# Kernel tuning notes

Hardware: AMD Instinct MI355X
Metric: run time of the kernel (lower is better)

Reference implementation:

```python
import jax, jax.numpy as jnp
import numpy as np
from jax import lax

S = 30      # num_sensors
FD = 200    # feature_dim
T = 1024    # signal length
B = 1024    # batch
NC = 7      # num_classes


def setup_inputs() -> dict:
    key = jax.random.key(0)
    ks = jax.random.split(key, 24)
    rn = lambda i, shape: jax.random.normal(ks[i], shape, jnp.float32) * 0.05
    # normalized adjacency with self-loops: D^-1/2 (A+I) D^-1/2
    rng = np.random.default_rng(0)
    A = (rng.random((S, S)) > 0.7).astype(np.float32)
    A = ((A + A.T) > 0).astype(np.float32)
    A_self = A + np.eye(S, dtype=np.float32)
    dinv = 1.0 / np.sqrt(A_self.sum(1))
    adj_self = jnp.asarray(dinv[:, None] * A_self * dinv[None, :])
    return dict(
        x=jax.random.normal(ks[0], (B, S, T), jnp.float32),
        adj_self=adj_self,
        Wc1=rn(1, (S, S, 3)), bc1=jnp.zeros((S,), jnp.float32),
        Wc2=rn(2, (S, S, 3)), bc2=jnp.zeros((S,), jnp.float32),
        Wt=rn(3, (T, FD)), bt=jnp.zeros((FD,), jnp.float32),
        Wa=rn(4, (FD, FD)),
        Wm1=rn(5, (FD, FD)), Wm2=rn(6, (FD, FD)), Wm3=rn(7, (FD, FD)),
        Wg1=rn(8, (FD, FD)), Wg2=rn(9, (FD, FD)),
        wg=rn(10, (FD, 3)),
        Wp1=rn(11, (FD, FD // 2)), Wp2=rn(12, (FD, FD // 2)), Wp3=rn(13, (FD, FD // 2)),
        Wl=rn(14, (FD, 150)), Wgl=rn(15, (FD, 150)),
        Ws1=rn(16, (S, S // 2)), Ws2=rn(17, (S // 2, S)),
        Wf1=rn(18, (300, 150)), Wf2=rn(19, (150, 300)),
        Wcls=rn(20, (S * 600, NC)), bcls=jnp.zeros((NC,), jnp.float32),
    )


def reference(x, adj_self, Wc1, bc1, Wc2, bc2, Wt, bt, Wa, Wm1, Wm2, Wm3,
              Wg1, Wg2, wg, Wp1, Wp2, Wp3, Wl, Wgl, Ws1, Ws2, Wf1, Wf2,
              Wcls, bcls):
    dn = ('NCH', 'OIH', 'NCH')
    # CNN feature extractor: [B,S,T] -> [B,S,FD]
    h = jax.nn.relu(lax.conv_general_dilated(x, Wc1, (1,), 'SAME', dimension_numbers=dn) + bc1[None, :, None])
    h = jax.nn.relu(lax.conv_general_dilated(h, Wc2, (1,), 'SAME', dimension_numbers=dn) + bc2[None, :, None])
    F2 = jax.nn.relu(jnp.einsum('bst,tf->bsf', h, Wt) + bt)
    # MGCN: learned feature adjacency + 3-order GCN (batched, replaces per-sample loop)
    A_F = jax.nn.softmax(jax.nn.relu(jnp.einsum('bif,fg,bjg->bij', F2, Wa, F2)), axis=-1)
    gc = lambda A, X, W: jax.nn.relu(jnp.einsum('bij,bjf,fg->big', A, X, W))
    x1 = gc(A_F, F2, Wm1)
    x2 = gc(A_F, x1, Wm2)
    x3 = gc(A_F, x2, Wm3)
    # signal GCN on physical adjacency (2-layer, eval mode so dropout is identity)
    h1 = jax.nn.relu(jnp.einsum('ij,bjf,fg->big', adj_self, F2, Wg1))
    x_sensor = jnp.einsum('ij,bjf,fg->big', adj_self, h1, Wg2)
    H1 = (x1 + x_sensor) * 0.5
    H2 = (x2 + x_sensor) * 0.5
    H3 = (x3 + x_sensor) * 0.5
    # adaptive aggregation: per-node softmax gate over 3 branches, project to FD//2 each -> 300
    scores = jnp.stack([jnp.einsum('bsf,f->bs', H, wg[:, k]) for k, H in enumerate((H1, H2, H3))], -1)
    g = jax.nn.softmax(scores, -1)  # [B,S,3]
    agg = lambda k, H, Wp: jnp.einsum('ij,bjf,fg->big', adj_self, g[..., k:k + 1] * H, Wp)
    G_h = jnp.concatenate([agg(0, H1, Wp1), agg(1, H2, Wp2), agg(2, H3, Wp3)], -1)  # [B,S,300]
    # LGFM: local (physical adj) + global (learned adj) -> 150+150
    loc = jax.nn.relu(jnp.einsum('ij,bjf,fg->big', adj_self, F2, Wl))
    glb = jax.nn.relu(jnp.einsum('bij,bjf,fg->big', A_F, F2, Wgl))
    G_v = jnp.concatenate([loc, glb], -1)  # [B,S,300]
    # cross squeeze-excitation: channel SE on G_h driven by G_v, feature SE on G_v driven by G_h
    wch = jax.nn.sigmoid(jax.nn.relu(G_v.mean(-1) @ Ws1) @ Ws2)   # [B,S]
    G_h_att = G_h * wch[:, :, None]
    wft = jax.nn.sigmoid(jax.nn.relu(G_h.mean(1) @ Wf1) @ Wf2)    # [B,300]
    G_v_att = G_v * wft[:, None, :]
    G = jnp.concatenate([G_h_att, G_v_att], -1).reshape(x.shape[0], -1)  # [B, S*600]
    return jax.nn.log_softmax(G @ Wcls + bcls, axis=-1)
```

## Files before the change

kernel.cpp:

```cpp
#include <hip/hip_runtime.h>
#include <math.h>

#define S   30
#define FD  200
#define TT  1024
#define BB  1024
#define NC  7

#define OFS_C1   0ull
#define OFS_F2   31457280ull
#define OFS_AF   0ull
#define OFS_GV   921600ull
#define OFS_GH   10137600ull
#define OFS_WCH  19353600ull
#define OFS_WFT  19384320ull
#define OFS_R    19691520ull

__global__ __launch_bounds__(256) void k_conv1(
    const float* __restrict__ x,
    const float* __restrict__ Wc1, const float* __restrict__ bc1,
    float* __restrict__ C1) {
    const int c = blockIdx.x, b = blockIdx.y;
    const int t = threadIdx.x;
    const int t0 = c * 256;
    __shared__ float xb[S * 258];
    __shared__ float w1l[90 * 32];
    for (int idx = t; idx < 2700; idx += 256) {
        int so = idx / 90, r = idx % 90;
        w1l[r * 32 + so] = Wc1[idx];
    }
    for (int idx = t; idx < 180; idx += 256) {
        int r = idx >> 1, z = idx & 1;
        w1l[r * 32 + 30 + z] = 0.f;
    }
    for (int idx = t; idx < S * 64; idx += 256) {
        int s = idx >> 6, u = idx & 63;
        float4 v = *(const float4*)(x + (size_t)(b * S + s) * TT + t0 + 4 * u);
        float* d = xb + s * 258 + 1 + 4 * u;
        d[0] = v.x; d[1] = v.y; d[2] = v.z; d[3] = v.w;
    }
    if (t < 60) {
        int s = t % S;
        if (t < S) {
            int gt = t0 - 1;
            xb[s * 258] = (gt >= 0) ? x[(size_t)(b * S + s) * TT + gt] : 0.f;
        } else {
            int gt = t0 + 256;
            xb[s * 258 + 257] = (gt < TT) ? x[(size_t)(b * S + s) * TT + gt] : 0.f;
        }
    }
    __syncthreads();
    float acc[32];
#pragma unroll
    for (int so = 0; so < 32; so++) acc[so] = (so < S) ? bc1[so] : 0.f;
    for (int si = 0; si < S; si++) {
        float v0 = xb[si * 258 + t];
        float v1 = xb[si * 258 + t + 1];
        float v2 = xb[si * 258 + t + 2];
        const float* wr = w1l + si * 96;
#pragma unroll
        for (int u = 0; u < 8; u++) {
            float4 w0 = *(const float4*)(wr + 4 * u);
            float4 w1 = *(const float4*)(wr + 32 + 4 * u);
            float4 w2 = *(const float4*)(wr + 64 + 4 * u);
            acc[4 * u + 0] = fmaf(w0.x, v0, fmaf(w1.x, v1, fmaf(w2.x, v2, acc[4 * u + 0])));
            acc[4 * u + 1] = fmaf(w0.y, v0, fmaf(w1.y, v1, fmaf(w2.y, v2, acc[4 * u + 1])));
            acc[4 * u + 2] = fmaf(w0.z, v0, fmaf(w1.z, v1, fmaf(w2.z, v2, acc[4 * u + 2])));
            acc[4 * u + 3] = fmaf(w0.w, v0, fmaf(w1.w, v1, fmaf(w2.w, v2, acc[4 * u + 3])));
        }
    }
#pragma unroll
    for (int so = 0; so < 32; so++) {
        if (so < S)
            C1[(size_t)(b * S + so) * TT + t0 + t] = fmaxf(acc[so], 0.f);
    }
}

#define FMA4(av, wv, accm)                           \
    {                                                \
        accm[0] = fmaf(av, (wv).x, accm[0]);         \
        accm[1] = fmaf(av, (wv).y, accm[1]);         \
        accm[2] = fmaf(av, (wv).z, accm[2]);         \
        accm[3] = fmaf(av, (wv).w, accm[3]);         \
    }

__device__ inline void fma_tile8(const float4 a0, const float4 a1,
                                 const float4 w[8], float accm[4]) {
    FMA4(a0.x, w[0], accm); FMA4(a0.y, w[1], accm);
    FMA4(a0.z, w[2], accm); FMA4(a0.w, w[3], accm);
    FMA4(a1.x, w[4], accm); FMA4(a1.y, w[5], accm);
    FMA4(a1.z, w[6], accm); FMA4(a1.w, w[7], accm);
}

template<int RPT>
__device__ inline void zacc(float acc[][4]) {
#pragma unroll
    for (int m = 0; m < RPT; m++)
#pragma unroll
        for (int q = 0; q < 4; q++) acc[m][q] = 0.f;
}

template<int RPT, int N, int K>
__device__ inline void gemm_w4_pf(const float* Xl, int xstr, const float* __restrict__ W,
                                  int ct, int rt, float acc[][4]) {
    const float* wp = W + 4 * ct;
    float4 wreg[8];
#pragma unroll
    for (int u = 0; u < 8; u++) wreg[u] = *(const float4*)(wp + u * N);
#pragma unroll 1
    for (int kt = 0; kt < K / 8 - 1; kt++) {
        float4 wnxt[8];
#pragma unroll
        for (int u = 0; u < 8; u++) wnxt[u] = *(const float4*)(wp + (kt * 8 + 8 + u) * N);
#pragma unroll
        for (int m = 0; m < RPT; m++) {
            const float* xr = Xl + (rt * RPT + m) * xstr + kt * 8;
            float4 a0 = *(const float4*)(xr);
            float4 a1 = *(const float4*)(xr + 4);
            fma_tile8(a0, a1, wreg, acc[m]);
        }
#pragma unroll
        for (int u = 0; u < 8; u++) wreg[u] = wnxt[u];
    }
    {
        const int kb = K - 8;
#pragma unroll
        for (int m = 0; m < RPT; m++) {
            const float* xr = Xl + (rt * RPT + m) * xstr + kb;
            float4 a0 = *(const float4*)(xr);
            float4 a1 = *(const float4*)(xr + 4);
            fma_tile8(a0, a1, wreg, acc[m]);
        }
    }
}

template<int RPT>
__device__ inline void gemm_a32(const float* Al, const float* Xl, int xstr,
                                int ct, int rt, float acc[][4]) {
#pragma unroll
    for (int k4 = 0; k4 < 8; k4++) {
        float4 xv0 = *(const float4*)(Xl + (4 * k4 + 0) * xstr + 4 * ct);
        float4 xv1 = *(const float4*)(Xl + (4 * k4 + 1) * xstr + 4 * ct);
        float4 xv2 = *(const float4*)(Xl + (4 * k4 + 2) * xstr + 4 * ct);
        float4 xv3 = *(const float4*)(Xl + (4 * k4 + 3) * xstr + 4 * ct);
#pragma unroll
        for (int m = 0; m < RPT; m++) {
            float4 av = *(const float4*)(Al + (rt * RPT + m) * 32 + 4 * k4);
            FMA4(av.x, xv0, acc[m]);
            FMA4(av.y, xv1, acc[m]);
            FMA4(av.z, xv2, acc[m]);
            FMA4(av.w, xv3, acc[m]);
        }
    }
}

__device__ inline void gemm_w150_pf(const float* Xl, const float* __restrict__ W,
                                    int ct2, int rt2, float acc[5][4], int off23) {
    const float* wp = W + 4 * ct2;
    float2 wa[8], wb[8];
#pragma unroll
    for (int u = 0; u < 8; u++) {
        wa[u] = *(const float2*)(wp + u * 150);
        wb[u] = *(const float2*)(wp + u * 150 + off23);
    }
#pragma unroll 1
    for (int kt = 0; kt < 24; kt++) {
        float2 na[8], nb[8];
#pragma unroll
        for (int u = 0; u < 8; u++) {
            int k = kt * 8 + 8 + u;
            na[u] = *(const float2*)(wp + k * 150);
            nb[u] = *(const float2*)(wp + k * 150 + off23);
        }
#pragma unroll
        for (int m = 0; m < 5; m++) {
            const float* xr = Xl + (rt2 * 5 + m) * FD + kt * 8;
            float4 a0 = *(const float4*)(xr);
            float4 a1 = *(const float4*)(xr + 4);
            float av[8] = {a0.x, a0.y, a0.z, a0.w, a1.x, a1.y, a1.z, a1.w};
#pragma unroll
            for (int u = 0; u < 8; u++) {
                acc[m][0] = fmaf(av[u], wa[u].x, acc[m][0]);
                acc[m][1] = fmaf(av[u], wa[u].y, acc[m][1]);
                acc[m][2] = fmaf(av[u], wb[u].x, acc[m][2]);
                acc[m][3] = fmaf(av[u], wb[u].y, acc[m][3]);
            }
        }
#pragma unroll
        for (int u = 0; u < 8; u++) { wa[u] = na[u]; wb[u] = nb[u]; }
    }
#pragma unroll
    for (int m = 0; m < 5; m++) {
        const float* xr = Xl + (rt2 * 5 + m) * FD + 192;
        float4 a0 = *(const float4*)(xr);
        float4 a1 = *(const float4*)(xr + 4);
        float av[8] = {a0.x, a0.y, a0.z, a0.w, a1.x, a1.y, a1.z, a1.w};
#pragma unroll
        for (int u = 0; u < 8; u++) {
            acc[m][0] = fmaf(av[u], wa[u].x, acc[m][0]);
            acc[m][1] = fmaf(av[u], wa[u].y, acc[m][1]);
            acc[m][2] = fmaf(av[u], wb[u].x, acc[m][2]);
            acc[m][3] = fmaf(av[u], wb[u].y, acc[m][3]);
        }
    }
}

__global__ __launch_bounds__(256) void k_f2(
    const float* __restrict__ C1,
    const float* __restrict__ Wc2, const float* __restrict__ bc2,
    const float* __restrict__ Wt, const float* __restrict__ bt,
    float* __restrict__ F2) {
    const int b = blockIdx.x, t = threadIdx.x;
    __shared__ float buf[S * 130];
    __shared__ float w2l[90 * 32];
    const int ct = t % 50, rt = t / 50;
    const int c3p = t & 63, sg = t >> 6;
    const int p0 = 2 * c3p;

    for (int idx = t; idx < 2700; idx += 256) {
        int ch = idx / 90, r = idx % 90;
        w2l[r * 32 + ch] = Wc2[idx];
    }
    for (int idx = t; idx < 180; idx += 256) {
        int r = idx >> 1, z = idx & 1;
        w2l[r * 32 + 30 + z] = 0.f;
    }
    float bias[8];
#pragma unroll
    for (int m = 0; m < 8; m++) {
        int ch = sg * 8 + m;
        bias[m] = bc2[ch < S ? ch : 0];
    }
    float acc[6][4];
    zacc<6>(acc);

    for (int ks = 0; ks < 8; ks++) {
        for (int idx = t; idx < S * 32; idx += 256) {
            int s = idx >> 5, u = idx & 31;
            float4 v = *(const float4*)(C1 + (size_t)(b * S + s) * TT + ks * 128 + 4 * u);
            float* d = buf + s * 130 + 1 + 4 * u;
            d[0] = v.x; d[1] = v.y; d[2] = v.z; d[3] = v.w;
        }
        if (t < 60) {
            int s = t % S;
            if (t < S) {
                int gt = ks * 128 - 1;
                buf[s * 130] = (gt >= 0) ? C1[(size_t)(b * S + s) * TT + gt] : 0.f;
            } else {
                int gt = ks * 128 + 128;
                buf[s * 130 + 129] = (gt < TT) ? C1[(size_t)(b * S + s) * TT + gt] : 0.f;
            }
        }
        __syncthreads();
        float a0[8], a1[8];
#pragma unroll
        for (int m = 0; m < 8; m++) { a0[m] = bias[m]; a1[m] = bias[m]; }
        for (int si = 0; si < S; si++) {
            float2 va = *(const float2*)(buf + si * 130 + p0);
            float2 vb = *(const float2*)(buf + si * 130 + p0 + 2);
            const float* wr = w2l + si * 96 + sg * 8;
            float4 w0a = *(const float4*)(wr);
            float4 w0b = *(const float4*)(wr + 4);
            float4 w1a = *(const float4*)(wr + 32);
            float4 w1b = *(const float4*)(wr + 36);
            float4 w2a = *(const float4*)(wr + 64);
            float4 w2b = *(const float4*)(wr + 68);
            float w0[8] = {w0a.x, w0a.y, w0a.z, w0a.w, w0b.x, w0b.y, w0b.z, w0b.w};
            float w1[8] = {w1a.x, w1a.y, w1a.z, w1a.w, w1b.x, w1b.y, w1b.z, w1b.w};
            float w2[8] = {w2a.x, w2a.y, w2a.z, w2a.w, w2b.x, w2b.y, w2b.z, w2b.w};
#pragma unroll
            for (int m = 0; m < 8; m++) {
                a0[m] = fmaf(w0[m], va.x, fmaf(w1[m], va.y, fmaf(w2[m], vb.x, a0[m])));
                a1[m] = fmaf(w0[m], va.y, fmaf(w1[m], vb.x, fmaf(w2[m], vb.y, a1[m])));
            }
        }
        __syncthreads();
#pragma unroll
        for (int m = 0; m < 8; m++) {
            int ch = sg * 8 + m;
            if (ch < S) {
                float2 o = {fmaxf(a0[m], 0.f), fmaxf(a1[m], 0.f)};
                *(float2*)(buf + ch * 128 + p0) = o;
            }
        }
        __syncthreads();
        if (t < 250)
            gemm_w4_pf<6, FD, 128>(buf, 128, Wt + (size_t)ks * 128 * FD, ct, rt, acc);
        __syncthreads();
    }
    if (t < 250) {
#pragma unroll
        for (int m = 0; m < 6; m++) {
            int row = rt * 6 + m;
            float4 o;
            o.x = fmaxf(acc[m][0] + bt[4 * ct + 0], 0.f);
            o.y = fmaxf(acc[m][1] + bt[4 * ct + 1], 0.f);
            o.z = fmaxf(acc[m][2] + bt[4 * ct + 2], 0.f);
            o.w = fmaxf(acc[m][3] + bt[4 * ct + 3], 0.f);
            *(float4*)(F2 + (size_t)(b * S + row) * FD + 4 * ct) = o;
        }
    }
}

__global__ __launch_bounds__(256) void k_att(
    const float* __restrict__ F2, const float* __restrict__ Wa,
    const float* __restrict__ adj, const float* __restrict__ Wl,
    const float* __restrict__ Wgl,
    float* __restrict__ AF, float* __restrict__ Gv) {
    const int b = blockIdx.x, t = threadIdx.x;
    __shared__ float A[32 * FD];
    __shared__ float Bu[32 * FD];
    __shared__ float scl[32 * 32];
    __shared__ float adjl[32 * 32];
    for (int idx = t; idx < 32 * FD; idx += 256) {
        A[idx] = (idx < S * FD) ? F2[(size_t)b * S * FD + idx] : 0.f;
        if (idx >= S * FD) Bu[idx] = 0.f;
    }
    for (int idx = t; idx < 1024; idx += 256) {
        int r = idx >> 5, cc = idx & 31;
        adjl[idx] = (r < S && cc < S) ? adj[r * S + cc] : 0.f;
        scl[idx] = 0.f;
    }
    __syncthreads();
    const int ct = t % 50, rt = t / 50;
    float acc[6][4];
    zacc<6>(acc);
    if (t < 250) {
        gemm_w4_pf<6, FD, FD>(A, FD, Wa, ct, rt, acc);
#pragma unroll
        for (int m = 0; m < 6; m++) {
            float4 o = {acc[m][0], acc[m][1], acc[m][2], acc[m][3]};
            *(float4*)(Bu + (rt * 6 + m) * FD + 4 * ct) = o;
        }
    }
    __syncthreads();
    for (int idx = t; idx < S * S; idx += 256) {
        int i = idx / S, j = idx % S;
        float a = 0.f;
        for (int f4 = 0; f4 < 50; f4++) {
            float4 p = *(const float4*)(Bu + i * FD + 4 * f4);
            float4 q = *(const float4*)(A + j * FD + 4 * f4);
            a = fmaf(p.x, q.x, a); a = fmaf(p.y, q.y, a);
            a = fmaf(p.z, q.z, a); a = fmaf(p.w, q.w, a);
        }
        scl[i * 32 + j] = fmaxf(a, 0.f);
    }
    __syncthreads();
    if (t < S) {
        float mx = -1e30f;
        for (int j = 0; j < S; j++) mx = fmaxf(mx, scl[t * 32 + j]);
        float den = 0.f;
        for (int j = 0; j < S; j++) den += expf(scl[t * 32 + j] - mx);
        float inv = 1.f / den;
        for (int j = 0; j < S; j++) scl[t * 32 + j] = expf(scl[t * 32 + j] - mx) * inv;
    }
    __syncthreads();
    for (int idx = t; idx < S * S; idx += 256)
        AF[(size_t)b * S * S + idx] = scl[(idx / S) * 32 + (idx % S)];
    zacc<6>(acc);
    if (t < 250) gemm_a32<6>(adjl, A, FD, ct, rt, acc);
    __syncthreads();
    if (t < 250)
#pragma unroll
        for (int m = 0; m < 6; m++) {
            float4 o = {acc[m][0], acc[m][1], acc[m][2], acc[m][3]};
            *(float4*)(Bu + (rt * 6 + m) * FD + 4 * ct) = o;
        }
    __syncthreads();
    const int ct2 = t % 38, rt2 = t / 38;
    const bool full = (4 * ct2 + 2) < 150;
    const int off23 = full ? 2 : -2;
    if (t < 228) {
        float a2[5][4];
        zacc<5>(a2);
        gemm_w150_pf(Bu, Wl, ct2, rt2, a2, off23);
#pragma unroll
        for (int m = 0; m < 5; m++) {
            float* o = Gv + (size_t)(b * S + rt2 * 5 + m) * 300 + 4 * ct2;
            o[0] = fmaxf(a2[m][0], 0.f); o[1] = fmaxf(a2[m][1], 0.f);
            if (full) { o[2] = fmaxf(a2[m][2], 0.f); o[3] = fmaxf(a2[m][3], 0.f); }
        }
    }
    __syncthreads();
    zacc<6>(acc);
    if (t < 250) gemm_a32<6>(scl, A, FD, ct, rt, acc);
    __syncthreads();
    if (t < 250)
#pragma unroll
        for (int m = 0; m < 6; m++) {
            float4 o = {acc[m][0], acc[m][1], acc[m][2], acc[m][3]};
            *(float4*)(Bu + (rt * 6 + m) * FD + 4 * ct) = o;
        }
    __syncthreads();
    if (t < 228) {
        float a2[5][4];
        zacc<5>(a2);
        gemm_w150_pf(Bu, Wgl, ct2, rt2, a2, off23);
#pragma unroll
        for (int m = 0; m < 5; m++) {
            float* o = Gv + (size_t)(b * S + rt2 * 5 + m) * 300 + 150 + 4 * ct2;
            o[0] = fmaxf(a2[m][0], 0.f); o[1] = fmaxf(a2[m][1], 0.f);
            if (full) { o[2] = fmaxf(a2[m][2], 0.f); o[3] = fmaxf(a2[m][3], 0.f); }
        }
    }
}

__global__ __launch_bounds__(256, 4) void k_mgcn(
    const float* __restrict__ F2g, const float* __restrict__ AFg,
    const float* __restrict__ adj,
    const float* __restrict__ Wg1, const float* __restrict__ Wg2,
    const float* __restrict__ Wm1, const float* __restrict__ Wm2,
    const float* __restrict__ Wm3, const float* __restrict__ wg,
    const float* __restrict__ Wp1, const float* __restrict__ Wp2,
    const float* __restrict__ Wp3,
    float* __restrict__ Rws, float* __restrict__ Gh) {
    const int b = blockIdx.x, t = threadIdx.x;
    __shared__ float A[32 * FD];
    __shared__ float afl[32 * 32];
    __shared__ float adjl[32 * 32];
    __shared__ float sk[96];
    __shared__ float gl[96];
    const int ct = t % 50, rt = t / 50;
    const int ct3 = t % 25, rt3 = t / 25;

    for (int idx = t; idx < 1500; idx += 256)
        *(float4*)(A + 4 * idx) = *(const float4*)(F2g + (size_t)b * S * FD + 4 * idx);
    for (int idx = t; idx < 400; idx += 256) A[6000 + idx] = 0.f;
    for (int idx = t; idx < 1024; idx += 256) {
        int r = idx >> 5, cc = idx & 31;
        afl[idx] = (r < S && cc < S) ? AFg[(size_t)b * S * S + r * S + cc] : 0.f;
        adjl[idx] = (r < S && cc < S) ? adj[r * S + cc] : 0.f;
    }
    if (t < 96) sk[t] = 0.f;
    __syncthreads();

    float acc[6][4];
    float xsr[6][4];

#define WRITE_ACC_A(RELU)                                                   \
    if (t < 250) {                                                          \
        _Pragma("unroll")                                                   \
        for (int m = 0; m < 6; m++) {                                       \
            float4 o;                                                       \
            o.x = RELU ? fmaxf(acc[m][0], 0.f) : acc[m][0];                 \
            o.y = RELU ? fmaxf(acc[m][1], 0.f) : acc[m][1];                 \
            o.z = RELU ? fmaxf(acc[m][2], 0.f) : acc[m][2];                 \
            o.w = RELU ? fmaxf(acc[m][3], 0.f) : acc[m][3];                 \
            *(float4*)(A + (rt * 6 + m) * FD + 4 * ct) = o;                 \
        }                                                                   \
    }

    zacc<6>(acc);
    if (t < 250) gemm_a32<6>(adjl, A, FD, ct, rt, acc);
    __syncthreads();
    WRITE_ACC_A(false);
    __syncthreads();
    zacc<6>(acc);
    if (t < 250) gemm_w4_pf<6, FD, FD>(A, FD, Wg1, ct, rt, acc);
    __syncthreads();
    WRITE_ACC_A(true);
    __syncthreads();
    zacc<6>(acc);
    if (t < 250) gemm_a32<6>(adjl, A, FD, ct, rt, acc);
    __syncthreads();
    WRITE_ACC_A(false);
    __syncthreads();
    zacc<6>(acc);
    if (t < 250) gemm_w4_pf<6, FD, FD>(A, FD, Wg2, ct, rt, acc);
    __syncthreads();
#pragma unroll
    for (int m = 0; m < 6; m++) {
#pragma unroll
        for (int q = 0; q < 4; q++) xsr[m][q] = acc[m][q];
    }
    for (int idx = t; idx < 1500; idx += 256)
        *(float4*)(A + 4 * idx) = *(const float4*)(F2g + (size_t)b * S * FD + 4 * idx);
    __syncthreads();

    const float* Wm[3] = {Wm1, Wm2, Wm3};
    const float* Wp[3] = {Wp1, Wp2, Wp3};
#pragma unroll 1
    for (int k = 0; k < 3; k++) {
        zacc<6>(acc);
        if (t < 250) gemm_a32<6>(afl, A, FD, ct, rt, acc);
        __syncthreads();
        WRITE_ACC_A(false);
        __syncthreads();
        zacc<6>(acc);
        if (t < 250) gemm_w4_pf<6, FD, FD>(A, FD, Wm[k], ct, rt, acc);
        __syncthreads();
        if (t < 250) {
#pragma unroll
            for (int m = 0; m < 6; m++) {
#pragma unroll
                for (int q = 0; q < 4; q++) acc[m][q] = fmaxf(acc[m][q], 0.f);
            }
#pragma unroll
            for (int m = 0; m < 6; m++) {
                int row = rt * 6 + m;
                float h0 = 0.5f * (acc[m][0] + xsr[m][0]);
                float h1 = 0.5f * (acc[m][1] + xsr[m][1]);
                float h2 = 0.5f * (acc[m][2] + xsr[m][2]);
                float h3 = 0.5f * (acc[m][3] + xsr[m][3]);
                float4 o = {h0, h1, h2, h3};
                *(float4*)(A + row * FD + 4 * ct) = o;
                float p = h0 * wg[(4 * ct + 0) * 3 + k]
                        + h1 * wg[(4 * ct + 1) * 3 + k]
                        + h2 * wg[(4 * ct + 2) * 3 + k]
                        + h3 * wg[(4 * ct + 3) * 3 + k];
                atomicAdd(&sk[row * 3 + k], p);
            }
        }
        __syncthreads();
        if (t < 250) {
            float a3[3][4];
            zacc<3>(a3);
            gemm_w4_pf<3, 100, FD>(A, FD, Wp[k], ct3, rt3, a3);
#pragma unroll
            for (int m = 0; m < 3; m++) {
                float4 o = {a3[m][0], a3[m][1], a3[m][2], a3[m][3]};
                *(float4*)(Rws + ((size_t)(k * BB + b) * S + rt3 * 3 + m) * 100 + 4 * ct3) = o;
            }
        }
        __syncthreads();
        if (k < 2) {
            WRITE_ACC_A(false);
            __syncthreads();
        }
    }

    if (t < S) {
        float a0 = sk[t * 3 + 0], a1 = sk[t * 3 + 1], a2 = sk[t * 3 + 2];
        float m = fmaxf(a0, fmaxf(a1, a2));
        float e0 = expf(a0 - m), e1 = expf(a1 - m), e2 = expf(a2 - m);
        float inv = 1.f / (e0 + e1 + e2);
        gl[t * 3 + 0] = e0 * inv; gl[t * 3 + 1] = e1 * inv; gl[t * 3 + 2] = e2 * inv;
    }
    __syncthreads();

#pragma unroll 1
    for (int k = 0; k < 3; k++) {
        for (int idx = t; idx < S * 100; idx += 256) {
            int row = idx / 100, col = idx % 100;
            A[row * FD + col] = Rws[((size_t)(k * BB + b) * S) * 100 + idx];
        }
        for (int idx = t; idx < 1024; idx += 256) {
            int cc = idx & 31;
            afl[idx] = (cc < S) ? adjl[idx] * gl[cc * 3 + k] : 0.f;
        }
        __syncthreads();
        if (t < 250) {
            float a3[3][4];
            zacc<3>(a3);
            gemm_a32<3>(afl, A, FD, ct3, rt3, a3);
#pragma unroll
            for (int m = 0; m < 3; m++) {
                float4 o = {a3[m][0], a3[m][1], a3[m][2], a3[m][3]};
                *(float4*)(Gh + (size_t)(b * S + rt3 * 3 + m) * 300 + k * 100 + 4 * ct3) = o;
            }
        }
        __syncthreads();
    }
#undef WRITE_ACC_A
}

__global__ __launch_bounds__(256) void k_se(const float* __restrict__ Gv, const float* __restrict__ Gh,
                                            const float* __restrict__ Ws1, const float* __restrict__ Ws2,
                                            const float* __restrict__ Wf1, const float* __restrict__ Wf2,
                                            float* __restrict__ wch, float* __restrict__ wft) {
    int b = blockIdx.x, t = threadIdx.x;
    __shared__ float mrow[S];
    __shared__ float u[15];
    __shared__ float mb[300];
    __shared__ float v[150];
    if (t < S) {
        float a = 0.f;
        const float* gp = Gv + ((size_t)b * S + t) * 300;
        for (int j = 0; j < 300; j++) a += gp[j];
        mrow[t] = a * (1.f / 300.f);
    }
    for (int j = t; j < 300; j += 256) {
        float a = 0.f;
        for (int s = 0; s < S; s++) a += Gh[(size_t)b * S * 300 + s * 300 + j];
        mb[j] = a * (1.f / S);
    }
    __syncthreads();
    if (t < 15) {
        float a = 0.f;
        for (int i = 0; i < S; i++) a += mrow[i] * Ws1[i * 15 + t];
        u[t] = fmaxf(a, 0.f);
    }
    if (t >= 64 && t < 64 + 150) {
        int h = t - 64;
        float a = 0.f;
        for (int j = 0; j < 300; j++) a += mb[j] * Wf1[j * 150 + h];
        v[h] = fmaxf(a, 0.f);
    }
    __syncthreads();
    if (t < S) {
        float a = 0.f;
        for (int h = 0; h < 15; h++) a += u[h] * Ws2[h * 30 + t];
        wch[b * S + t] = 1.f / (1.f + expf(-a));
    }
    for (int j = t; j < 300; j += 256) {
        float a = 0.f;
        for (int h = 0; h < 150; h++) a += v[h] * Wf2[h * 300 + j];
        wft[b * 300 + j] = 1.f / (1.f + expf(-a));
    }
}

__global__ __launch_bounds__(256) void k_cls(const float* __restrict__ Gh, const float* __restrict__ Gv,
                                             const float* __restrict__ wch, const float* __restrict__ wft,
                                             const float* __restrict__ Wcls, const float* __restrict__ bcls,
                                             float* __restrict__ out) {
    const int b = blockIdx.x, t = threadIdx.x;
    __shared__ float red[NC][256];
    __shared__ float wftl[300];
    __shared__ float wchl[S];
    for (int j = t; j < 300; j += 256) wftl[j] = wft[(size_t)b * 300 + j];
    if (t < S) wchl[t] = wch[b * S + t];
    __syncthreads();
    float acc[NC];
#pragma unroll
    for (int c = 0; c < NC; c++) acc[c] = 0.f;
    for (int i = t; i < S * 600; i += 256) {
        int s = i / 600, j = i % 600;
        float gval = (j < 300)
            ? Gh[(size_t)b * S * 300 + s * 300 + j] * wchl[s]
            : Gv[(size_t)b * S * 300 + s * 300 + (j - 300)] * wftl[j - 300];
        const float* wr = Wcls + (size_t)i * NC;
#pragma unroll
        for (int c = 0; c < NC; c++) acc[c] = fmaf(gval, wr[c], acc[c]);
    }
#pragma unroll
    for (int c = 0; c < NC; c++) red[c][t] = acc[c];
    __syncthreads();
    for (int off = 128; off > 0; off >>= 1) {
        if (t < off) {
#pragma unroll
            for (int c = 0; c < NC; c++) red[c][t] += red[c][t + off];
        }
        __syncthreads();
    }
    if (t == 0) {
        float lg[NC];
        float mx = -1e30f;
#pragma unroll
        for (int c = 0; c < NC; c++) { lg[c] = red[c][0] + bcls[c]; mx = fmaxf(mx, lg[c]); }
        float den = 0.f;
#pragma unroll
        for (int c = 0; c < NC; c++) den += expf(lg[c] - mx);
        float lden = logf(den) + mx;
#pragma unroll
        for (int c = 0; c < NC; c++) out[b * NC + c] = lg[c] - lden;
    }
}

extern "C" void kernel_launch(void* const* d_in, const int* in_sizes, int n_in,
                              void* d_out, int out_size, void* d_ws, size_t ws_size,
                              hipStream_t stream) {
    const float* x    = (const float*)d_in[0];
    const float* adj  = (const float*)d_in[1];
    const float* Wc1  = (const float*)d_in[2];
    const float* bc1  = (const float*)d_in[3];
    const float* Wc2  = (const float*)d_in[4];
    const float* bc2  = (const float*)d_in[5];
    const float* Wt   = (const float*)d_in[6];
    const float* bt   = (const float*)d_in[7];
    const float* Wa   = (const float*)d_in[8];
    const float* Wm1  = (const float*)d_in[9];
    const float* Wm2  = (const float*)d_in[10];
    const float* Wm3  = (const float*)d_in[11];
    const float* Wg1  = (const float*)d_in[12];
    const float* Wg2  = (const float*)d_in[13];
    const float* wg   = (const float*)d_in[14];
    const float* Wp1  = (const float*)d_in[15];
    const float* Wp2  = (const float*)d_in[16];
    const float* Wp3  = (const float*)d_in[17];
    const float* Wl   = (const float*)d_in[18];
    const float* Wgl  = (const float*)d_in[19];
    const float* Ws1  = (const float*)d_in[20];
    const float* Ws2  = (const float*)d_in[21];
    const float* Wf1  = (const float*)d_in[22];
    const float* Wf2  = (const float*)d_in[23];
    const float* Wcls = (const float*)d_in[24];
    const float* bcls = (const float*)d_in[25];

    float* ws  = (float*)d_ws;
    float* C1  = ws + OFS_C1;
    float* F2  = ws + OFS_F2;
    float* AF  = ws + OFS_AF;
    float* GV  = ws + OFS_GV;
    float* GH  = ws + OFS_GH;
    float* WCH = ws + OFS_WCH;
    float* WFT = ws + OFS_WFT;
    float* RWS = ws + OFS_R;
    float* out = (float*)d_out;

    k_conv1<<<dim3(4, BB), 256, 0, stream>>>(x, Wc1, bc1, C1);
    k_f2<<<BB, 256, 0, stream>>>(C1, Wc2, bc2, Wt, bt, F2);
    k_att<<<BB, 256, 0, stream>>>(F2, Wa, adj, Wl, Wgl, AF, GV);
    k_mgcn<<<BB, 256, 0, stream>>>(F2, AF, adj, Wg1, Wg2, Wm1, Wm2, Wm3, wg,
                                   Wp1, Wp2, Wp3, RWS, GH);
    k_se<<<BB, 256, 0, stream>>>(GV, GH, Ws1, Ws2, Wf1, Wf2, WCH, WFT);
    k_cls<<<BB, 256, 0, stream>>>(GH, GV, WCH, WFT, Wcls, bcls, out);
}
```

Measured before the change: 1.148 ms.

## Process two batch samples per block in k_mgcn to share weight loads

k_mgcn now handles two batch samples per workgroup, with dual GEMM helpers that load each weight tile from global memory once and apply it to both samples' LDS activations. The grid is halved and the launch bound drops from 4 to 2 blocks per CU to leave room for the doubled accumulators. The goal is to halve weight traffic and synchronisation overhead per sample. The cost is doubled LDS use per block (about 55KB) and higher register pressure, which lowers occupancy and could cause spills.

```diff
diff --git a/kernel.cpp b/kernel.cpp
--- a/kernel.cpp
+++ b/kernel.cpp
@@ -134,6 +134,56 @@
     }
 }
 
+template<int RPT, int N, int K>
+__device__ inline void gemm_w4_pf_dual(const float* X0, const float* X1, int xstr,
+                                       const float* __restrict__ W,
+                                       int ct, int rt,
+                                       float acc0[][4], float acc1[][4]) {
+    const float* wp = W + 4 * ct;
+    float4 wreg[8];
+#pragma unroll
+    for (int u = 0; u < 8; u++) wreg[u] = *(const float4*)(wp + u * N);
+#pragma unroll 1
+    for (int kt = 0; kt < K / 8 - 1; kt++) {
+        float4 wnxt[8];
+#pragma unroll
+        for (int u = 0; u < 8; u++) wnxt[u] = *(const float4*)(wp + (kt * 8 + 8 + u) * N);
+#pragma unroll
+        for (int m = 0; m < RPT; m++) {
+            const float* xr = X0 + (rt * RPT + m) * xstr + kt * 8;
+            float4 a0 = *(const float4*)(xr);
+            float4 a1 = *(const float4*)(xr + 4);
+            fma_tile8(a0, a1, wreg, acc0[m]);
+        }
+#pragma unroll
+        for (int m = 0; m < RPT; m++) {
+            const float* xr = X1 + (rt * RPT + m) * xstr + kt * 8;
+            float4 a0 = *(const float4*)(xr);
+            float4 a1 = *(const float4*)(xr + 4);
+            fma_tile8(a0, a1, wreg, acc1[m]);
+        }
+#pragma unroll
+        for (int u = 0; u < 8; u++) wreg[u] = wnxt[u];
+    }
+    {
+        const int kb = K - 8;
+#pragma unroll
+        for (int m = 0; m < RPT; m++) {
+            const float* xr = X0 + (rt * RPT + m) * xstr + kb;
+            float4 a0 = *(const float4*)(xr);
+            float4 a1 = *(const float4*)(xr + 4);
+            fma_tile8(a0, a1, wreg, acc0[m]);
+        }
+#pragma unroll
+        for (int m = 0; m < RPT; m++) {
+            const float* xr = X1 + (rt * RPT + m) * xstr + kb;
+            float4 a0 = *(const float4*)(xr);
+            float4 a1 = *(const float4*)(xr + 4);
+            fma_tile8(a0, a1, wreg, acc1[m]);
+        }
+    }
+}
+
 template<int RPT>
 __device__ inline void gemm_a32(const float* Al, const float* Xl, int xstr,
                                 int ct, int rt, float acc[][4]) {
@@ -150,6 +200,37 @@
             FMA4(av.y, xv1, acc[m]);
             FMA4(av.z, xv2, acc[m]);
             FMA4(av.w, xv3, acc[m]);
+        }
+    }
+}
+
+template<int RPT>
+__device__ inline void gemm_a32_dual(const float* Al0, const float* X0,
+                                     const float* Al1, const float* X1,
+                                     int xstr, int ct, int rt,
+                                     float acc0[][4], float acc1[][4]) {
+#pragma unroll
+    for (int k4 = 0; k4 < 8; k4++) {
+        float4 x00 = *(const float4*)(X0 + (4 * k4 + 0) * xstr + 4 * ct);
+        float4 x01 = *(const float4*)(X0 + (4 * k4 + 1) * xstr + 4 * ct);
+        float4 x02 = *(const float4*)(X0 + (4 * k4 + 2) * xstr + 4 * ct);
+        float4 x03 = *(const float4*)(X0 + (4 * k4 + 3) * xstr + 4 * ct);
+        float4 x10 = *(const float4*)(X1 + (4 * k4 + 0) * xstr + 4 * ct);
+        float4 x11 = *(const float4*)(X1 + (4 * k4 + 1) * xstr + 4 * ct);
+        float4 x12 = *(const float4*)(X1 + (4 * k4 + 2) * xstr + 4 * ct);
+        float4 x13 = *(const float4*)(X1 + (4 * k4 + 3) * xstr + 4 * ct);
+#pragma unroll
+        for (int m = 0; m < RPT; m++) {
+            float4 av0 = *(const float4*)(Al0 + (rt * RPT + m) * 32 + 4 * k4);
+            FMA4(av0.x, x00, acc0[m]);
+            FMA4(av0.y, x01, acc0[m]);
+            FMA4(av0.z, x02, acc0[m]);
+            FMA4(av0.w, x03, acc0[m]);
+            float4 av1 = *(const float4*)(Al1 + (rt * RPT + m) * 32 + 4 * k4);
+            FMA4(av1.x, x10, acc1[m]);
+            FMA4(av1.y, x11, acc1[m]);
+            FMA4(av1.z, x12, acc1[m]);
+            FMA4(av1.w, x13, acc1[m]);
         }
     }
 }
@@ -405,7 +486,7 @@
     }
 }
 
-__global__ __launch_bounds__(256, 4) void k_mgcn(
+__global__ __launch_bounds__(256, 2) void k_mgcn(
     const float* __restrict__ F2g, const float* __restrict__ AFg,
     const float* __restrict__ adj,
     const float* __restrict__ Wg1, const float* __restrict__ Wg2,
@@ -414,117 +495,141 @@
     const float* __restrict__ Wp1, const float* __restrict__ Wp2,
     const float* __restrict__ Wp3,
     float* __restrict__ Rws, float* __restrict__ Gh) {
-    const int b = blockIdx.x, t = threadIdx.x;
-    __shared__ float A[32 * FD];
-    __shared__ float afl[32 * 32];
-    __shared__ float adjl[32 * 32];
-    __shared__ float sk[96];
-    __shared__ float gl[96];
+    const int b0 = blockIdx.x * 2, b1 = b0 + 1;
+    const int t = threadIdx.x;
+    __shared__ float A0[32 * FD], A1[32 * FD];
+    __shared__ float afl0[1024], afl1[1024];
+    __shared__ float adjl[1024];
+    __shared__ float sk[192];
+    __shared__ float gl[192];
     const int ct = t % 50, rt = t / 50;
     const int ct3 = t % 25, rt3 = t / 25;
 
-    for (int idx = t; idx < 1500; idx += 256)
-        *(float4*)(A + 4 * idx) = *(const float4*)(F2g + (size_t)b * S * FD + 4 * idx);
-    for (int idx = t; idx < 400; idx += 256) A[6000 + idx] = 0.f;
+    for (int idx = t; idx < 1500; idx += 256) {
+        *(float4*)(A0 + 4 * idx) = *(const float4*)(F2g + (size_t)b0 * S * FD + 4 * idx);
+        *(float4*)(A1 + 4 * idx) = *(const float4*)(F2g + (size_t)b1 * S * FD + 4 * idx);
+    }
+    for (int idx = t; idx < 400; idx += 256) { A0[6000 + idx] = 0.f; A1[6000 + idx] = 0.f; }
     for (int idx = t; idx < 1024; idx += 256) {
         int r = idx >> 5, cc = idx & 31;
-        afl[idx] = (r < S && cc < S) ? AFg[(size_t)b * S * S + r * S + cc] : 0.f;
-        adjl[idx] = (r < S && cc < S) ? adj[r * S + cc] : 0.f;
-    }
-    if (t < 96) sk[t] = 0.f;
-    __syncthreads();
-
-    float acc[6][4];
-    float xsr[6][4];
-
-#define WRITE_ACC_A(RELU)                                                   \
+        bool in = (r < S && cc < S);
+        afl0[idx] = in ? AFg[(size_t)b0 * S * S + r * S + cc] : 0.f;
+        afl1[idx] = in ? AFg[(size_t)b1 * S * S + r * S + cc] : 0.f;
+        adjl[idx] = in ? adj[r * S + cc] : 0.f;
+    }
+    if (t < 192) sk[t] = 0.f;
+    __syncthreads();
+
+    float acc0[6][4], acc1[6][4], xsr0[6][4], xsr1[6][4];
+
+#define DZ() { zacc<6>(acc0); zacc<6>(acc1); }
+#define DWRITE(RELU)                                                        \
     if (t < 250) {                                                          \
         _Pragma("unroll")                                                   \
         for (int m = 0; m < 6; m++) {                                       \
-            float4 o;                                                       \
-            o.x = RELU ? fmaxf(acc[m][0], 0.f) : acc[m][0];                 \
-            o.y = RELU ? fmaxf(acc[m][1], 0.f) : acc[m][1];                 \
-            o.z = RELU ? fmaxf(acc[m][2], 0.f) : acc[m][2];                 \
-            o.w = RELU ? fmaxf(acc[m][3], 0.f) : acc[m][3];                 \
-            *(float4*)(A + (rt * 6 + m) * FD + 4 * ct) = o;                 \
+            float4 o0, o1;                                                  \
+            o0.x = RELU ? fmaxf(acc0[m][0], 0.f) : acc0[m][0];              \
+            o0.y = RELU ? fmaxf(acc0[m][1], 0.f) : acc0[m][1];              \
+            o0.z = RELU ? fmaxf(acc0[m][2], 0.f) : acc0[m][2];              \
+            o0.w = RELU ? fmaxf(acc0[m][3], 0.f) : acc0[m][3];              \
+            o1.x = RELU ? fmaxf(acc1[m][0], 0.f) : acc1[m][0];              \
+            o1.y = RELU ? fmaxf(acc1[m][1], 0.f) : acc1[m][1];              \
+            o1.z = RELU ? fmaxf(acc1[m][2], 0.f) : acc1[m][2];              \
+            o1.w = RELU ? fmaxf(acc1[m][3], 0.f) : acc1[m][3];              \
+            *(float4*)(A0 + (rt * 6 + m) * FD + 4 * ct) = o0;               \
+            *(float4*)(A1 + (rt * 6 + m) * FD + 4 * ct) = o1;               \
         }                                                                   \
     }
 
-    zacc<6>(acc);
-    if (t < 250) gemm_a32<6>(adjl, A, FD, ct, rt, acc);
-    __syncthreads();
-    WRITE_ACC_A(false);
-    __syncthreads();
-    zacc<6>(acc);
-    if (t < 250) gemm_w4_pf<6, FD, FD>(A, FD, Wg1, ct, rt, acc);
-    __syncthreads();
-    WRITE_ACC_A(true);
-    __syncthreads();
-    zacc<6>(acc);
-    if (t < 250) gemm_a32<6>(adjl, A, FD, ct, rt, acc);
-    __syncthreads();
-    WRITE_ACC_A(false);
-    __syncthreads();
-    zacc<6>(acc);
-    if (t < 250) gemm_w4_pf<6, FD, FD>(A, FD, Wg2, ct, rt, acc);
+    DZ();
+    if (t < 250) gemm_a32_dual<6>(adjl, A0, adjl, A1, FD, ct, rt, acc0, acc1);
+    __syncthreads();
+    DWRITE(false);
+    __syncthreads();
+    DZ();
+    if (t < 250) gemm_w4_pf_dual<6, FD, FD>(A0, A1, FD, Wg1, ct, rt, acc0, acc1);
+    __syncthreads();
+    DWRITE(true);
+    __syncthreads();
+    DZ();
+    if (t < 250) gemm_a32_dual<6>(adjl, A0, adjl, A1, FD, ct, rt, acc0, acc1);
+    __syncthreads();
+    DWRITE(false);
+    __syncthreads();
+    DZ();
+    if (t < 250) gemm_w4_pf_dual<6, FD, FD>(A0, A1, FD, Wg2, ct, rt, acc0, acc1);
     __syncthreads();
 #pragma unroll
     for (int m = 0; m < 6; m++) {
 #pragma unroll
-        for (int q = 0; q < 4; q++) xsr[m][q] = acc[m][q];
-    }
-    for (int idx = t; idx < 1500; idx += 256)
-        *(float4*)(A + 4 * idx) = *(const float4*)(F2g + (size_t)b * S * FD + 4 * idx);
+        for (int q = 0; q < 4; q++) { xsr0[m][q] = acc0[m][q]; xsr1[m][q] = acc1[m][q]; }
+    }
+    for (int idx = t; idx < 1500; idx += 256) {
+        *(float4*)(A0 + 4 * idx) = *(const float4*)(F2g + (size_t)b0 * S * FD + 4 * idx);
+        *(float4*)(A1 + 4 * idx) = *(const float4*)(F2g + (size_t)b1 * S * FD + 4 * idx);
+    }
     __syncthreads();
 
     const float* Wm[3] = {Wm1, Wm2, Wm3};
     const float* Wp[3] = {Wp1, Wp2, Wp3};
 #pragma unroll 1
     for (int k = 0; k < 3; k++) {
-        zacc<6>(acc);
-        if (t < 250) gemm_a32<6>(afl, A, FD, ct, rt, acc);
-        __syncthreads();
-        WRITE_ACC_A(false);
-        __syncthreads();
-        zacc<6>(acc);
-        if (t < 250) gemm_w4_pf<6, FD, FD>(A, FD, Wm[k], ct, rt, acc);
+        DZ();
+        if (t < 250) gemm_a32_dual<6>(afl0, A0, afl1, A1, FD, ct, rt, acc0, acc1);
+        __syncthreads();
+        DWRITE(false);
+        __syncthreads();
+        DZ();
+        if (t < 250) gemm_w4_pf_dual<6, FD, FD>(A0, A1, FD, Wm[k], ct, rt, acc0, acc1);
         __syncthreads();
         if (t < 250) {
 #pragma unroll
             for (int m = 0; m < 6; m++) {
 #pragma unroll
-                for (int q = 0; q < 4; q++) acc[m][q] = fmaxf(acc[m][q], 0.f);
+                for (int q = 0; q < 4; q++) {
+                    acc0[m][q] = fmaxf(acc0[m][q], 0.f);
+                    acc1[m][q] = fmaxf(acc1[m][q], 0.f);
+                }
             }
 #pragma unroll
             for (int m = 0; m < 6; m++) {
                 int row = rt * 6 + m;
-                float h0 = 0.5f * (acc[m][0] + xsr[m][0]);
-                float h1 = 0.5f * (acc[m][1] + xsr[m][1]);
-                float h2 = 0.5f * (acc[m][2] + xsr[m][2]);
-                float h3 = 0.5f * (acc[m][3] + xsr[m][3]);
-                float4 o = {h0, h1, h2, h3};
-                *(float4*)(A + row * FD + 4 * ct) = o;
-                float p = h0 * wg[(4 * ct + 0) * 3 + k]
-                        + h1 * wg[(4 * ct + 1) * 3 + k]
-                        + h2 * wg[(4 * ct + 2) * 3 + k]
-                        + h3 * wg[(4 * ct + 3) * 3 + k];
-                atomicAdd(&sk[row * 3 + k], p);
+                float wg0 = wg[(4 * ct + 0) * 3 + k], wg1v = wg[(4 * ct + 1) * 3 + k];
+                float wg2v = wg[(4 * ct + 2) * 3 + k], wg3 = wg[(4 * ct + 3) * 3 + k];
+                float h00 = 0.5f * (acc0[m][0] + xsr0[m][0]);
+                float h01 = 0.5f * (acc0[m][1] + xsr0[m][1]);
+                float h02 = 0.5f * (acc0[m][2] + xsr0[m][2]);
+                float h03 = 0.5f * (acc0[m][3] + xsr0[m][3]);
+                float4 o0 = {h00, h01, h02, h03};
+                *(float4*)(A0 + row * FD + 4 * ct) = o0;
+                atomicAdd(&sk[row * 3 + k],
+                          h00 * wg0 + h01 * wg1v + h02 * wg2v + h03 * wg3);
+                float h10 = 0.5f * (acc1[m][0] + xsr1[m][0]);
+                float h11 = 0.5f * (acc1[m][1] + xsr1[m][1]);
+                float h12 = 0.5f * (acc1[m][2] + xsr1[m][2]);
+                float h13 = 0.5f * (acc1[m][3] + xsr1[m][3]);
+                float4 o1 = {h10, h11, h12, h13};
+                *(float4*)(A1 + row * FD + 4 * ct) = o1;
+                atomicAdd(&sk[96 + row * 3 + k],
+                          h10 * wg0 + h11 * wg1v + h12 * wg2v + h13 * wg3);
             }
         }
         __syncthreads();
         if (t < 250) {
-            float a3[3][4];
-            zacc<3>(a3);
-            gemm_w4_pf<3, 100, FD>(A, FD, Wp[k], ct3, rt3, a3);
+            float a30[3][4], a31[3][4];
+            zacc<3>(a30); zacc<3>(a31);
+            gemm_w4_pf_dual<3, 100, FD>(A0, A1, FD, Wp[k], ct3, rt3, a30, a31);
 #pragma unroll
             for (int m = 0; m < 3; m++) {
-                float4 o = {a3[m][0], a3[m][1], a3[m][2], a3[m][3]};
-                *(float4*)(Rws + ((size_t)(k * BB + b) * S + rt3 * 3 + m) * 100 + 4 * ct3) = o;
+                float4 o0 = {a30[m][0], a30[m][1], a30[m][2], a30[m][3]};
+                float4 o1 = {a31[m][0], a31[m][1], a31[m][2], a31[m][3]};
+                *(float4*)(Rws + ((size_t)(k * BB + b0) * S + rt3 * 3 + m) * 100 + 4 * ct3) = o0;
+                *(float4*)(Rws + ((size_t)(k * BB + b1) * S + rt3 * 3 + m) * 100 + 4 * ct3) = o1;
             }
         }
         __syncthreads();
         if (k < 2) {
-            WRITE_ACC_A(false);
+            DWRITE(false);
             __syncthreads();
         }
     }
@@ -535,6 +640,13 @@
         float e0 = expf(a0 - m), e1 = expf(a1 - m), e2 = expf(a2 - m);
         float inv = 1.f / (e0 + e1 + e2);
         gl[t * 3 + 0] = e0 * inv; gl[t * 3 + 1] = e1 * inv; gl[t * 3 + 2] = e2 * inv;
+    } else if (t >= 64 && t < 64 + S) {
+        int s = t - 64;
+        float a0 = sk[96 + s * 3 + 0], a1 = sk[96 + s * 3 + 1], a2 = sk[96 + s * 3 + 2];
+        float m = fmaxf(a0, fmaxf(a1, a2));
+        float e0 = expf(a0 - m), e1 = expf(a1 - m), e2 = expf(a2 - m);
+        float inv = 1.f / (e0 + e1 + e2);
+        gl[96 + s * 3 + 0] = e0 * inv; gl[96 + s * 3 + 1] = e1 * inv; gl[96 + s * 3 + 2] = e2 * inv;
     }
     __syncthreads();
 
@@ -542,26 +654,31 @@
     for (int k = 0; k < 3; k++) {
         for (int idx = t; idx < S * 100; idx += 256) {
             int row = idx / 100, col = idx % 100;
-            A[row * FD + col] = Rws[((size_t)(k * BB + b) * S) * 100 + idx];
+            A0[row * FD + col] = Rws[((size_t)(k * BB + b0) * S) * 100 + idx];
+            A1[row * FD + col] = Rws[((size_t)(k * BB + b1) * S) * 100 + idx];
         }
         for (int idx = t; idx < 1024; idx += 256) {
             int cc = idx & 31;
-            afl[idx] = (cc < S) ? adjl[idx] * gl[cc * 3 + k] : 0.f;
+            afl0[idx] = (cc < S) ? adjl[idx] * gl[cc * 3 + k] : 0.f;
+            afl1[idx] = (cc < S) ? adjl[idx] * gl[96 + cc * 3 + k] : 0.f;
         }
         __syncthreads();
         if (t < 250) {
-            float a3[3][4];
-            zacc<3>(a3);
-            gemm_a32<3>(afl, A, FD, ct3, rt3, a3);
+            float a30[3][4], a31[3][4];
+            zacc<3>(a30); zacc<3>(a31);
+            gemm_a32_dual<3>(afl0, A0, afl1, A1, FD, ct3, rt3, a30, a31);
 #pragma unroll
             for (int m = 0; m < 3; m++) {
-                float4 o = {a3[m][0], a3[m][1], a3[m][2], a3[m][3]};
-                *(float4*)(Gh + (size_t)(b * S + rt3 * 3 + m) * 300 + k * 100 + 4 * ct3) = o;
+                float4 o0 = {a30[m][0], a30[m][1], a30[m][2], a30[m][3]};
+                float4 o1 = {a31[m][0], a31[m][1], a31[m][2], a31[m][3]};
+                *(float4*)(Gh + (size_t)(b0 * S + rt3 * 3 + m) * 300 + k * 100 + 4 * ct3) = o0;
+                *(float4*)(Gh + (size_t)(b1 * S + rt3 * 3 + m) * 300 + k * 100 + 4 * ct3) = o1;
             }
         }
         __syncthreads();
     }
-#undef WRITE_ACC_A
+#undef DZ
+#undef DWRITE
 }
 
 __global__ __launch_bounds__(256) void k_se(const float* __restrict__ Gv, const float* __restrict__ Gh,
@@ -700,8 +817,8 @@
     k_conv1<<<dim3(4, BB), 256, 0, stream>>>(x, Wc1, bc1, C1);
     k_f2<<<BB, 256, 0, stream>>>(C1, Wc2, bc2, Wt, bt, F2);
     k_att<<<BB, 256, 0, stream>>>(F2, Wa, adj, Wl, Wgl, AF, GV);
-    k_mgcn<<<BB, 256, 0, stream>>>(F2, AF, adj, Wg1, Wg2, Wm1, Wm2, Wm3, wg,
-                                   Wp1, Wp2, Wp3, RWS, GH);
+    k_mgcn<<<BB / 2, 256, 0, stream>>>(F2, AF, adj, Wg1, Wg2, Wm1, Wm2, Wm3, wg,
+                                       Wp1, Wp2, Wp3, RWS, GH);
     k_se<<<BB, 256, 0, stream>>>(GV, GH, Ws1, Ws2, Wf1, Wf2, WCH, WFT);
     k_cls<<<BB, 256, 0, stream>>>(GH, GV, WCH, WFT, Wcls, bcls, out);
 }
```

Result: no change. 1.145 ms (-0.2%).
